# Optimization experiments

Measured on AMD Instinct MI355X. Metric: run time of the kernel, lower is better.

The kernel has to match this reference:

```python
import jax, jax.numpy as jnp
import numpy as np

SCALING = 2.0  # alpha / r = 128 / 64


def setup_inputs() -> dict:
    key = jax.random.key(0)
    k1, k2, k3, k4, k5 = jax.random.split(key, 5)
    B, S, DIN, DOUT, R = 4, 2048, 4096, 4096, 64
    x = jax.random.normal(k1, (B, S, DIN), dtype=jnp.float32)
    # int8 quantized weight codes in [-127, 127] (stored as int32 for portability)
    qweight = jax.random.randint(k2, (DOUT, DIN), -127, 128, dtype=jnp.int32)
    # per-output-row absmax dequant scale (already divided by 127)
    scale = jax.random.uniform(k3, (DOUT, 1), dtype=jnp.float32, minval=0.005, maxval=0.02)
    lora_A = jax.random.normal(k4, (R, DIN), dtype=jnp.float32) * 0.02
    lora_B = jax.random.normal(k5, (DOUT, R), dtype=jnp.float32) * 0.02
    return {"x": x, "qweight": qweight, "scale": scale, "lora_A": lora_A, "lora_B": lora_B}


def reference(x, qweight, scale, lora_A, lora_B):
    # inline int8 dequant: w[o,i] = code[o,i] * scale[o]
    w = qweight.astype(x.dtype) * scale  # [DOUT, DIN]
    base = jnp.einsum('bsi,oi->bso', x, w)
    # low-rank LoRA path: (x @ A^T) @ B^T, scaled
    xa = jnp.einsum('bsi,ri->bsr', x, lora_A)       # [B,S,R]
    lora = jnp.einsum('bsr,or->bso', xa, lora_B)    # [B,S,DOUT]
    return base + SCALING * lora
```

## Files before the change

### kernel.cpp

```cpp
#include <hip/hip_runtime.h>
#include <hip/hip_bf16.h>
#include <stdint.h>


typedef __bf16 bf16x8 __attribute__((ext_vector_type(8)));
typedef float f32x4 __attribute__((ext_vector_type(4)));
typedef int i32x4 __attribute__((ext_vector_type(4)));

#define DIN   4096
#define DOUT  4096
#define MTOT  8192
#define RNK   64
#define NT    64

__device__ inline void gload_lds16(const void* g, void* l) {
  __builtin_amdgcn_global_load_lds((const __attribute__((address_space(1))) void*)g,
                                   (__attribute__((address_space(3))) void*)l,
                                   16, 0, 0);
}

__global__ __launch_bounds__(256) void prep_kernel(const float* __restrict__ x,
                                                   const int* __restrict__ qw,
                                                   const float* __restrict__ lA,
                                                   const float* __restrict__ lB,
                                                   signed char* __restrict__ Xi8,
                                                   float* __restrict__ tstep,
                                                   signed char* __restrict__ Wi8,
                                                   signed char* __restrict__ Ai8,
                                                   float* __restrict__ astep,
                                                   __bf16* __restrict__ Blt) {
  const int bid = blockIdx.x, t = threadIdx.x;
  const float* src = nullptr;
  signed char* dst = nullptr;
  float* stp = nullptr;
  int row = 0;
  if (bid < 8192) { src = x; dst = Xi8; stp = tstep; row = bid; }
  else if (bid < 8256) { src = lA; dst = Ai8; stp = astep; row = bid - 8192; }
  if (src) {
    const float4* xr = (const float4*)(src + (size_t)row * DIN);
    float4 v[4];
    float m = 0.f;
#pragma unroll
    for (int s = 0; s < 4; ++s) {
      v[s] = xr[t + s * 256];
      m = fmaxf(m, fmaxf(fmaxf(fabsf(v[s].x), fabsf(v[s].y)),
                         fmaxf(fabsf(v[s].z), fabsf(v[s].w))));
    }
#pragma unroll
    for (int off = 32; off > 0; off >>= 1) m = fmaxf(m, __shfl_xor(m, off));
    __shared__ float wm[4];
    if ((t & 63) == 0) wm[t >> 6] = m;
    __syncthreads();
    m = fmaxf(fmaxf(wm[0], wm[1]), fmaxf(wm[2], wm[3]));
    m = fmaxf(m, 1e-30f);
    const float rs = 127.0f / m;
    int* orow = (int*)(dst + (size_t)row * DIN);
#pragma unroll
    for (int s = 0; s < 4; ++s) {
      float e[4] = {v[s].x, v[s].y, v[s].z, v[s].w};
      union { signed char c[4]; int i; } p;
#pragma unroll
      for (int j = 0; j < 4; ++j) {
        int q = __float2int_rn(e[j] * rs);
        q = q > 127 ? 127 : (q < -127 ? -127 : q);
        p.c[j] = (signed char)q;
      }
      orow[t + s * 256] = p.i;
    }
    if (t == 0) stp[row] = m * (1.0f / 127.0f);
  } else if (bid < 8512) {
    int i = (bid - 8256) * 256 + t;
    float4 v = ((const float4*)lB)[i];
    union { __bf16 h[4]; uint64_t u; } p;
    p.h[0] = (__bf16)(2.0f * v.x); p.h[1] = (__bf16)(2.0f * v.y);
    p.h[2] = (__bf16)(2.0f * v.z); p.h[3] = (__bf16)(2.0f * v.w);
    ((uint64_t*)Blt)[i] = p.u;
  } else {
    int i = (bid - 8512) * 256 + t;
    int4 v = ((const int4*)qw)[i];
    union { signed char c[4]; int i; } p;
    p.c[0] = (signed char)v.x; p.c[1] = (signed char)v.y;
    p.c[2] = (signed char)v.z; p.c[3] = (signed char)v.w;
    ((int*)Wi8)[i] = p.i;
  }
}

__global__ __launch_bounds__(256) void lora_xa_kernel(const signed char* __restrict__ Xi8,
                                                      const float* __restrict__ tstep,
                                                      const signed char* __restrict__ Ai8,
                                                      const float* __restrict__ astep,
                                                      __bf16* __restrict__ xa) {
  __shared__ i32x4 red[4][64][4];
  const int w = threadIdx.x >> 6, lane = threadIdx.x & 63;
  const int rowbase = blockIdx.x * 16;
  i32x4 acc[4] = {};
  const int k00 = w * 1024 + (lane >> 4) * 16;
  const signed char* xrow = Xi8 + (size_t)(rowbase + (lane & 15)) * DIN + k00;
  const signed char* ab = Ai8 + (size_t)(lane & 15) * DIN + k00;
#pragma unroll 4
  for (int k = 0; k < 1024; k += 64) {
    i32x4 af = *(const i32x4*)(xrow + k);
#pragma unroll
    for (int ni = 0; ni < 4; ++ni) {
      i32x4 bv = *(const i32x4*)(ab + (size_t)ni * 16 * DIN + k);
      acc[ni] = __builtin_amdgcn_mfma_i32_16x16x64_i8(af, bv, acc[ni], 0, 0, 0);
    }
  }
#pragma unroll
  for (int ni = 0; ni < 4; ++ni) red[w][lane][ni] = acc[ni];
  __syncthreads();
  if (w == 0) {
    f32x4 tm = *(const f32x4*)&tstep[rowbase + (lane >> 4) * 4];
#pragma unroll
    for (int ni = 0; ni < 4; ++ni) {
      i32x4 s = red[0][lane][ni];
#pragma unroll
      for (int u = 1; u < 4; ++u) s += red[u][lane][ni];
      const int col = ni * 16 + (lane & 15);
      const float as = astep[col];
#pragma unroll
      for (int j = 0; j < 4; ++j) {
        int row = rowbase + (lane >> 4) * 4 + j;
        xa[(size_t)row * RNK + col] = (__bf16)((float)s[j] * tm[j] * as);
      }
    }
  }
}

__global__ __launch_bounds__(512, 1) void gemm_i8_kernel(const signed char* __restrict__ Xi8,
                                                         const signed char* __restrict__ Wi8,
                                                         const float* __restrict__ scale,
                                                         const float* __restrict__ tstep,
                                                         const __bf16* __restrict__ xa,
                                                         const __bf16* __restrict__ Blt,
                                                         float* __restrict__ out) {
  extern __shared__ char smem[];
  const int tid = threadIdx.x;
  const int lane = tid & 63;
  const int w = tid >> 6;
  const int wr = w >> 2;
  const int wc = w & 3;

  const int swz = (blockIdx.x & 7) * 64 + (blockIdx.x >> 3);
  const int bx = swz & 15;
  const int by = swz >> 4;
  const size_t bm = (size_t)by * 256, bn = (size_t)bx * 256;

  const int rc = ((lane >> 4) ^ ((lane >> 1) & 3)) << 4;
  const int srow = tid >> 2;
  const int scol = ((tid & 3) ^ ((tid >> 3) & 3)) << 4;

  auto SH = [&](const signed char* g, size_t r0, int srct, int ldsoff) {
    gload_lds16(g + (r0 + srow) * (size_t)4096 + srct * 64 + scol,
                smem + ldsoff + tid * 16);
  };
  auto stage = [&](int srct, int buf) {
    int b = buf * 32768;
    SH(Xi8, bm, srct, b); SH(Xi8, bm + 128, srct, b + 8192);
    SH(Wi8, bn, srct, b + 16384); SH(Wi8, bn + 128, srct, b + 24576);
  };

  i32x4 aP[4], bP[4], aQ[4], bQ[4], a2[4];
  i32x4 acc[8][4] = {};

  stage(0, 0); stage(1, 1); stage(2, 2);
  asm volatile("s_waitcnt vmcnt(4)" ::: "memory");
  __builtin_amdgcn_s_barrier();
  {
    const int ab0 = wr * 8192 + (lane & 15) * 64 + rc;
    const int bb0 = 16384 + (wc >> 1) * 8192 + (wc & 1) * 4096 + (lane & 15) * 64 + rc;
#pragma unroll
    for (int mi = 0; mi < 4; ++mi) aP[mi] = *(const i32x4*)(smem + ab0 + mi * 1024);
#pragma unroll
    for (int ni = 0; ni < 4; ++ni) bP[ni] = *(const i32x4*)(smem + bb0 + ni * 1024);
  }

  auto body = [&](int kt, auto& ac, auto& bc, auto& an, auto& bn) {
    const int bufb = (kt & 3) * 32768;
    const int ab = bufb + wr * 8192 + (lane & 15) * 64 + rc;
    const int st = (kt + 3 < NT) ? kt + 3 : NT - 1;
    stage(st, (kt + 3) & 3);
#pragma unroll
    for (int mi = 0; mi < 4; ++mi)
      a2[mi] = *(const i32x4*)(smem + ab + 4096 + mi * 1024);
#pragma unroll
    for (int mi = 0; mi < 4; ++mi)
#pragma unroll
      for (int ni = 0; ni < 4; ++ni)
        acc[mi][ni] = __builtin_amdgcn_mfma_i32_16x16x64_i8(ac[mi], bc[ni], acc[mi][ni], 0, 0, 0);
    const int nbufb = ((kt + 1) & 3) * 32768;
    const int nab = nbufb + wr * 8192 + (lane & 15) * 64 + rc;
    const int nbb = nbufb + 16384 + (wc >> 1) * 8192 + (wc & 1) * 4096 + (lane & 15) * 64 + rc;
#pragma unroll
    for (int mi = 0; mi < 4; ++mi) an[mi] = *(const i32x4*)(smem + nab + mi * 1024);
#pragma unroll
    for (int ni = 0; ni < 4; ++ni) bn[ni] = *(const i32x4*)(smem + nbb + ni * 1024);
#pragma unroll
    for (int mi = 0; mi < 4; ++mi)
#pragma unroll
      for (int ni = 0; ni < 4; ++ni)
        acc[4 + mi][ni] = __builtin_amdgcn_mfma_i32_16x16x64_i8(a2[mi], bc[ni], acc[4 + mi][ni], 0, 0, 0);
    __builtin_amdgcn_sched_barrier(0);
    asm volatile("s_waitcnt vmcnt(4)" ::: "memory");
    __builtin_amdgcn_s_barrier();
  };

  for (int kt = 0; kt < NT; kt += 2) {
    body(kt, aP, bP, aQ, bQ);
    body(kt + 1, aQ, bQ, aP, bP);
  }

  const int sl_row = lane >> 3;
  const int sl_col = ((lane & 7) ^ (lane >> 3)) << 4;
  auto SBF = [&](const __bf16* g, size_t r0, int ldsoff) {
    char* d0 = smem + ldsoff + w * 2048 + lane * 16;
#pragma unroll
    for (int s = 0; s < 2; ++s) {
      const int rl = (w * 2 + s) * 8 + sl_row;
      gload_lds16((const char*)g + (r0 + rl) * 128 + sl_col, d0 + s * 1024);
    }
  };
  SBF(xa, bm, 0); SBF(xa, bm + 128, 16384);
  SBF(Blt, bn, 32768); SBF(Blt, bn + 128, 49152);

  float sc[4];
#pragma unroll
  for (int ni = 0; ni < 4; ++ni)
    sc[ni] = scale[bn + wc * 64 + ni * 16 + (lane & 15)];
  f32x4 tm[8];
#pragma unroll
  for (int mi = 0; mi < 8; ++mi)
    tm[mi] = *(const f32x4*)&tstep[bm + wr * 128 + mi * 16 + (lane >> 4) * 4];

  asm volatile("s_waitcnt vmcnt(0)" ::: "memory");
  __builtin_amdgcn_s_barrier();

  const int cx0 = ((lane >> 4) << 4) ^ ((lane & 7) << 4);
  const int cx1 = (64 | ((lane >> 4) << 4)) ^ ((lane & 7) << 4);
  const int abE = wr * 16384 + (lane & 15) * 128;
  const int bbE = 32768 + (wc >> 1) * 16384 + ((wc & 1) * 64 + (lane & 15)) * 128;

  bf16x8 bl0[4], bl1[4];
#pragma unroll
  for (int ni = 0; ni < 4; ++ni) {
    bl0[ni] = *(const bf16x8*)(smem + bbE + ni * 2048 + cx0);
    bl1[ni] = *(const bf16x8*)(smem + bbE + ni * 2048 + cx1);
  }
#pragma unroll
  for (int mi = 0; mi < 8; ++mi) {
    bf16x8 ax0 = *(const bf16x8*)(smem + abE + mi * 2048 + cx0);
    bf16x8 ax1 = *(const bf16x8*)(smem + abE + mi * 2048 + cx1);
    const size_t row = bm + wr * 128 + mi * 16 + (lane >> 4) * 4;
#pragma unroll
    for (int ni = 0; ni < 4; ++ni) {
      f32x4 l = {0.f, 0.f, 0.f, 0.f};
      l = __builtin_amdgcn_mfma_f32_16x16x32_bf16(ax0, bl0[ni], l, 0, 0, 0);
      l = __builtin_amdgcn_mfma_f32_16x16x32_bf16(ax1, bl1[ni], l, 0, 0, 0);
      const size_t col = bn + wc * 64 + ni * 16 + (lane & 15);
#pragma unroll
      for (int j = 0; j < 4; ++j)
        out[(row + j) * DOUT + col] = (float)acc[mi][ni][j] * (sc[ni] * tm[mi][j]) + l[j];
    }
  }
}

extern "C" void kernel_launch(void* const* d_in, const int* in_sizes, int n_in,
                              void* d_out, int out_size, void* d_ws, size_t ws_size,
                              hipStream_t stream) {
  const float* x = (const float*)d_in[0];
  const int* qw = (const int*)d_in[1];
  const float* scale = (const float*)d_in[2];
  const float* lA = (const float*)d_in[3];
  const float* lB = (const float*)d_in[4];
  float* out = (float*)d_out;

  char* ws = (char*)d_ws;
  signed char* Xi8 = (signed char*)ws;
  signed char* Wi8 = (signed char*)(ws + 33554432);
  __bf16* xa    = (__bf16*)(ws + 50331648);
  signed char* Ai8 = (signed char*)(ws + 51380224);
  __bf16* Blt   = (__bf16*)(ws + 51904512);
  float* tstep  = (float*)(ws + 52428800);
  float* astep  = (float*)(ws + 52461568);

  hipFuncSetAttribute((const void*)gemm_i8_kernel,
                      hipFuncAttributeMaxDynamicSharedMemorySize, 131072);

  prep_kernel<<<24896, 256, 0, stream>>>(x, qw, lA, lB, Xi8, tstep, Wi8, Ai8, astep, Blt);
  lora_xa_kernel<<<MTOT / 16, 256, 0, stream>>>(Xi8, tstep, Ai8, astep, xa);
  gemm_i8_kernel<<<(MTOT / 256) * (DOUT / 256), 512, 131072, stream>>>(
      Xi8, Wi8, scale, tstep, xa, Blt, out);
}
```

Measured before the change: 198.9 us.

## Halve GEMM workgroup to four waves, each computing a 128x128 tile

The int8 GEMM kernel drops from 8 waves to 4 waves per 256x256 block. Each wave now holds an 8x8 grid of 16x16 int32 accumulators (128x128 outputs). The LDS staging loop and the epilogue LoRA fragment loads are reorganised to match. This raises MFMA work per LDS fragment load and cuts the number of waves at the barrier. In exchange it needs far more accumulator registers, which risks spills or AGPR pressure, and leaves fewer waves to hide latency.

```diff
diff --git a/kernel.cpp b/kernel.cpp
--- a/kernel.cpp
+++ b/kernel.cpp
@@ -127,7 +127,7 @@
   }
 }
 
-__global__ __launch_bounds__(512, 1) void gemm_i8_kernel(const signed char* __restrict__ Xi8,
+__global__ __launch_bounds__(256, 1) void gemm_i8_kernel(const signed char* __restrict__ Xi8,
                                                          const signed char* __restrict__ Wi8,
                                                          const float* __restrict__ scale,
                                                          const float* __restrict__ tstep,
@@ -138,8 +138,8 @@
   const int tid = threadIdx.x;
   const int lane = tid & 63;
   const int w = tid >> 6;
-  const int wr = w >> 2;
-  const int wc = w & 3;
+  const int wr = w >> 1;
+  const int wc = w & 1;
 
   const int swz = (blockIdx.x & 7) * 64 + (blockIdx.x >> 3);
   const int bx = swz & 15;
@@ -150,58 +150,50 @@
   const int srow = tid >> 2;
   const int scol = ((tid & 3) ^ ((tid >> 3) & 3)) << 4;
 
-  auto SH = [&](const signed char* g, size_t r0, int srct, int ldsoff) {
-    gload_lds16(g + (r0 + srow) * (size_t)4096 + srct * 64 + scol,
-                smem + ldsoff + tid * 16);
-  };
   auto stage = [&](int srct, int buf) {
     int b = buf * 32768;
-    SH(Xi8, bm, srct, b); SH(Xi8, bm + 128, srct, b + 8192);
-    SH(Wi8, bn, srct, b + 16384); SH(Wi8, bn + 128, srct, b + 24576);
+#pragma unroll
+    for (int i = 0; i < 4; ++i)
+      gload_lds16(Xi8 + (bm + 64 * i + srow) * (size_t)4096 + srct * 64 + scol,
+                  smem + b + i * 4096 + tid * 16);
+#pragma unroll
+    for (int i = 0; i < 4; ++i)
+      gload_lds16(Wi8 + (bn + 64 * i + srow) * (size_t)4096 + srct * 64 + scol,
+                  smem + b + 16384 + i * 4096 + tid * 16);
   };
 
-  i32x4 aP[4], bP[4], aQ[4], bQ[4], a2[4];
-  i32x4 acc[8][4] = {};
+  const int aoff = wr * 8192 + (lane & 15) * 64 + rc;
+  const int boff = 16384 + wc * 8192 + (lane & 15) * 64 + rc;
+
+  i32x4 aP[8], bP[8], aQ[8], bQ[8];
+  i32x4 acc[8][8] = {};
 
   stage(0, 0); stage(1, 1); stage(2, 2);
-  asm volatile("s_waitcnt vmcnt(4)" ::: "memory");
+  asm volatile("s_waitcnt vmcnt(8)" ::: "memory");
   __builtin_amdgcn_s_barrier();
-  {
-    const int ab0 = wr * 8192 + (lane & 15) * 64 + rc;
-    const int bb0 = 16384 + (wc >> 1) * 8192 + (wc & 1) * 4096 + (lane & 15) * 64 + rc;
-#pragma unroll
-    for (int mi = 0; mi < 4; ++mi) aP[mi] = *(const i32x4*)(smem + ab0 + mi * 1024);
-#pragma unroll
-    for (int ni = 0; ni < 4; ++ni) bP[ni] = *(const i32x4*)(smem + bb0 + ni * 1024);
-  }
-
-  auto body = [&](int kt, auto& ac, auto& bc, auto& an, auto& bn) {
-    const int bufb = (kt & 3) * 32768;
-    const int ab = bufb + wr * 8192 + (lane & 15) * 64 + rc;
+#pragma unroll
+  for (int mi = 0; mi < 8; ++mi) aP[mi] = *(const i32x4*)(smem + aoff + mi * 1024);
+#pragma unroll
+  for (int ni = 0; ni < 8; ++ni) bP[ni] = *(const i32x4*)(smem + boff + ni * 1024);
+
+  auto body = [&](int kt, i32x4 (&aC)[8], i32x4 (&bC)[8],
+                  i32x4 (&aN)[8], i32x4 (&bN)[8]) {
     const int st = (kt + 3 < NT) ? kt + 3 : NT - 1;
     stage(st, (kt + 3) & 3);
-#pragma unroll
-    for (int mi = 0; mi < 4; ++mi)
-      a2[mi] = *(const i32x4*)(smem + ab + 4096 + mi * 1024);
-#pragma unroll
-    for (int mi = 0; mi < 4; ++mi)
-#pragma unroll
-      for (int ni = 0; ni < 4; ++ni)
-        acc[mi][ni] = __builtin_amdgcn_mfma_i32_16x16x64_i8(ac[mi], bc[ni], acc[mi][ni], 0, 0, 0);
-    const int nbufb = ((kt + 1) & 3) * 32768;
-    const int nab = nbufb + wr * 8192 + (lane & 15) * 64 + rc;
-    const int nbb = nbufb + 16384 + (wc >> 1) * 8192 + (wc & 1) * 4096 + (lane & 15) * 64 + rc;
-#pragma unroll
-    for (int mi = 0; mi < 4; ++mi) an[mi] = *(const i32x4*)(smem + nab + mi * 1024);
-#pragma unroll
-    for (int ni = 0; ni < 4; ++ni) bn[ni] = *(const i32x4*)(smem + nbb + ni * 1024);
-#pragma unroll
-    for (int mi = 0; mi < 4; ++mi)
-#pragma unroll
-      for (int ni = 0; ni < 4; ++ni)
-        acc[4 + mi][ni] = __builtin_amdgcn_mfma_i32_16x16x64_i8(a2[mi], bc[ni], acc[4 + mi][ni], 0, 0, 0);
+    if (kt + 1 < NT) {
+      const int nb = ((kt + 1) & 3) * 32768;
+#pragma unroll
+      for (int mi = 0; mi < 8; ++mi) aN[mi] = *(const i32x4*)(smem + nb + aoff + mi * 1024);
+#pragma unroll
+      for (int ni = 0; ni < 8; ++ni) bN[ni] = *(const i32x4*)(smem + nb + boff + ni * 1024);
+    }
+#pragma unroll
+    for (int mi = 0; mi < 8; ++mi)
+#pragma unroll
+      for (int ni = 0; ni < 8; ++ni)
+        acc[mi][ni] = __builtin_amdgcn_mfma_i32_16x16x64_i8(aC[mi], bC[ni], acc[mi][ni], 0, 0, 0);
     __builtin_amdgcn_sched_barrier(0);
-    asm volatile("s_waitcnt vmcnt(4)" ::: "memory");
+    asm volatile("s_waitcnt vmcnt(8)" ::: "memory");
     __builtin_amdgcn_s_barrier();
   };
 
@@ -210,23 +202,23 @@
     body(kt + 1, aQ, bQ, aP, bP);
   }
 
-  const int sl_row = lane >> 3;
-  const int sl_col = ((lane & 7) ^ (lane >> 3)) << 4;
-  auto SBF = [&](const __bf16* g, size_t r0, int ldsoff) {
-    char* d0 = smem + ldsoff + w * 2048 + lane * 16;
-#pragma unroll
-    for (int s = 0; s < 2; ++s) {
-      const int rl = (w * 2 + s) * 8 + sl_row;
-      gload_lds16((const char*)g + (r0 + rl) * 128 + sl_col, d0 + s * 1024);
-    }
-  };
-  SBF(xa, bm, 0); SBF(xa, bm + 128, 16384);
-  SBF(Blt, bn, 32768); SBF(Blt, bn + 128, 49152);
-
-  float sc[4];
-#pragma unroll
-  for (int ni = 0; ni < 4; ++ni)
-    sc[ni] = scale[bn + wc * 64 + ni * 16 + (lane & 15)];
+  asm volatile("s_waitcnt vmcnt(0)" ::: "memory");
+  __builtin_amdgcn_s_barrier();
+  const int erow = tid >> 3;
+  const int ecol = (((tid & 7) ^ ((tid >> 3) & 7)) << 4);
+#pragma unroll
+  for (int i = 0; i < 8; ++i)
+    gload_lds16((const char*)xa + (bm + 32 * i + erow) * 128 + ecol,
+                smem + i * 4096 + tid * 16);
+#pragma unroll
+  for (int i = 0; i < 8; ++i)
+    gload_lds16((const char*)Blt + (bn + 32 * i + erow) * 128 + ecol,
+                smem + 32768 + i * 4096 + tid * 16);
+
+  float sc[8];
+#pragma unroll
+  for (int ni = 0; ni < 8; ++ni)
+    sc[ni] = scale[bn + wc * 128 + ni * 16 + (lane & 15)];
   f32x4 tm[8];
 #pragma unroll
   for (int mi = 0; mi < 8; ++mi)
@@ -238,25 +230,21 @@
   const int cx0 = ((lane >> 4) << 4) ^ ((lane & 7) << 4);
   const int cx1 = (64 | ((lane >> 4) << 4)) ^ ((lane & 7) << 4);
   const int abE = wr * 16384 + (lane & 15) * 128;
-  const int bbE = 32768 + (wc >> 1) * 16384 + ((wc & 1) * 64 + (lane & 15)) * 128;
-
-  bf16x8 bl0[4], bl1[4];
-#pragma unroll
-  for (int ni = 0; ni < 4; ++ni) {
-    bl0[ni] = *(const bf16x8*)(smem + bbE + ni * 2048 + cx0);
-    bl1[ni] = *(const bf16x8*)(smem + bbE + ni * 2048 + cx1);
-  }
+  const int bbE = 32768 + wc * 16384 + (lane & 15) * 128;
+
 #pragma unroll
   for (int mi = 0; mi < 8; ++mi) {
     bf16x8 ax0 = *(const bf16x8*)(smem + abE + mi * 2048 + cx0);
     bf16x8 ax1 = *(const bf16x8*)(smem + abE + mi * 2048 + cx1);
     const size_t row = bm + wr * 128 + mi * 16 + (lane >> 4) * 4;
 #pragma unroll
-    for (int ni = 0; ni < 4; ++ni) {
+    for (int ni = 0; ni < 8; ++ni) {
+      bf16x8 bl0 = *(const bf16x8*)(smem + bbE + ni * 2048 + cx0);
+      bf16x8 bl1 = *(const bf16x8*)(smem + bbE + ni * 2048 + cx1);
       f32x4 l = {0.f, 0.f, 0.f, 0.f};
-      l = __builtin_amdgcn_mfma_f32_16x16x32_bf16(ax0, bl0[ni], l, 0, 0, 0);
-      l = __builtin_amdgcn_mfma_f32_16x16x32_bf16(ax1, bl1[ni], l, 0, 0, 0);
-      const size_t col = bn + wc * 64 + ni * 16 + (lane & 15);
+      l = __builtin_amdgcn_mfma_f32_16x16x32_bf16(ax0, bl0, l, 0, 0, 0);
+      l = __builtin_amdgcn_mfma_f32_16x16x32_bf16(ax1, bl1, l, 0, 0, 0);
+      const size_t col = bn + wc * 128 + ni * 16 + (lane & 15);
 #pragma unroll
       for (int j = 0; j < 4; ++j)
         out[(row + j) * DOUT + col] = (float)acc[mi][ni][j] * (sc[ni] * tm[mi][j]) + l[j];
@@ -288,6 +276,6 @@
 
   prep_kernel<<<24896, 256, 0, stream>>>(x, qw, lA, lB, Xi8, tstep, Wi8, Ai8, astep, Blt);
   lora_xa_kernel<<<MTOT / 16, 256, 0, stream>>>(Xi8, tstep, Ai8, astep, xa);
-  gemm_i8_kernel<<<(MTOT / 256) * (DOUT / 256), 512, 131072, stream>>>(
+  gemm_i8_kernel<<<(MTOT / 256) * (DOUT / 256), 256, 131072, stream>>>(
       Xi8, Wi8, scale, tstep, xa, Blt, out);
 }
```

Result: slower. 615.0 us (+209.2%).

## Defer upper-half MFMAs to next iteration to overlap LDS operand loads

Applied to the files above, without the earlier changes.

Restructures the int8 GEMM main loop into a skewed software pipeline. The second block of MFMAs for each k-tile now runs at the start of the next iteration, so the LDS reads of the next tile's A/B fragments and the upper-half A fragments are issued before the lower-half MFMAs rather than between them. It adds a second register set for the upper A fragments, an explicit lgkmcnt(0) wait, a prologue and epilogue iteration, and a final vmcnt(0) barrier before the LoRA stage. The extra registers may raise VGPR pressure and affect occupancy.

```diff
diff --git a/kernel.cpp b/kernel.cpp
--- a/kernel.cpp
+++ b/kernel.cpp
@@ -160,55 +160,68 @@
     SH(Wi8, bn, srct, b + 16384); SH(Wi8, bn + 128, srct, b + 24576);
   };
 
-  i32x4 aP[4], bP[4], aQ[4], bQ[4], a2[4];
+  const int aoffw = wr * 8192 + (lane & 15) * 64 + rc;
+  const int boffw = 16384 + (wc >> 1) * 8192 + (wc & 1) * 4096 + (lane & 15) * 64 + rc;
+
+  i32x4 aP[4], bP[4], aQ[4], bQ[4], a2P[4], a2Q[4];
   i32x4 acc[8][4] = {};
 
   stage(0, 0); stage(1, 1); stage(2, 2);
   asm volatile("s_waitcnt vmcnt(4)" ::: "memory");
   __builtin_amdgcn_s_barrier();
-  {
-    const int ab0 = wr * 8192 + (lane & 15) * 64 + rc;
-    const int bb0 = 16384 + (wc >> 1) * 8192 + (wc & 1) * 4096 + (lane & 15) * 64 + rc;
-#pragma unroll
-    for (int mi = 0; mi < 4; ++mi) aP[mi] = *(const i32x4*)(smem + ab0 + mi * 1024);
-#pragma unroll
-    for (int ni = 0; ni < 4; ++ni) bP[ni] = *(const i32x4*)(smem + bb0 + ni * 1024);
-  }
-
-  auto body = [&](int kt, auto& ac, auto& bc, auto& an, auto& bn) {
-    const int bufb = (kt & 3) * 32768;
-    const int ab = bufb + wr * 8192 + (lane & 15) * 64 + rc;
+#pragma unroll
+  for (int mi = 0; mi < 4; ++mi) aP[mi] = *(const i32x4*)(smem + aoffw + mi * 1024);
+#pragma unroll
+  for (int ni = 0; ni < 4; ++ni) bP[ni] = *(const i32x4*)(smem + boffw + ni * 1024);
+
+  auto body = [&](int kt, i32x4 (&AY)[4], i32x4 (&BY)[4],
+                  i32x4 (&AX)[4], i32x4 (&BX)[4],
+                  i32x4 (&a2Y)[4], i32x4 (&a2X)[4], bool doHi) {
+    if (doHi) {
+#pragma unroll
+      for (int mi = 0; mi < 4; ++mi)
+#pragma unroll
+        for (int ni = 0; ni < 4; ++ni)
+          acc[4 + mi][ni] = __builtin_amdgcn_mfma_i32_16x16x64_i8(a2X[mi], BX[ni], acc[4 + mi][ni], 0, 0, 0);
+    }
     const int st = (kt + 3 < NT) ? kt + 3 : NT - 1;
     stage(st, (kt + 3) & 3);
+    const int ab = (kt & 3) * 32768 + aoffw;
 #pragma unroll
     for (int mi = 0; mi < 4; ++mi)
-      a2[mi] = *(const i32x4*)(smem + ab + 4096 + mi * 1024);
+      a2Y[mi] = *(const i32x4*)(smem + ab + 4096 + mi * 1024);
+    if (kt + 1 < NT) {
+      const int nb = ((kt + 1) & 3) * 32768;
+#pragma unroll
+      for (int mi = 0; mi < 4; ++mi) AX[mi] = *(const i32x4*)(smem + nb + aoffw + mi * 1024);
+#pragma unroll
+      for (int ni = 0; ni < 4; ++ni) BX[ni] = *(const i32x4*)(smem + nb + boffw + ni * 1024);
+    }
 #pragma unroll
     for (int mi = 0; mi < 4; ++mi)
 #pragma unroll
       for (int ni = 0; ni < 4; ++ni)
-        acc[mi][ni] = __builtin_amdgcn_mfma_i32_16x16x64_i8(ac[mi], bc[ni], acc[mi][ni], 0, 0, 0);
-    const int nbufb = ((kt + 1) & 3) * 32768;
-    const int nab = nbufb + wr * 8192 + (lane & 15) * 64 + rc;
-    const int nbb = nbufb + 16384 + (wc >> 1) * 8192 + (wc & 1) * 4096 + (lane & 15) * 64 + rc;
-#pragma unroll
-    for (int mi = 0; mi < 4; ++mi) an[mi] = *(const i32x4*)(smem + nab + mi * 1024);
-#pragma unroll
-    for (int ni = 0; ni < 4; ++ni) bn[ni] = *(const i32x4*)(smem + nbb + ni * 1024);
-#pragma unroll
-    for (int mi = 0; mi < 4; ++mi)
-#pragma unroll
-      for (int ni = 0; ni < 4; ++ni)
-        acc[4 + mi][ni] = __builtin_amdgcn_mfma_i32_16x16x64_i8(a2[mi], bc[ni], acc[4 + mi][ni], 0, 0, 0);
+        acc[mi][ni] = __builtin_amdgcn_mfma_i32_16x16x64_i8(AY[mi], BY[ni], acc[mi][ni], 0, 0, 0);
+    asm volatile("s_waitcnt lgkmcnt(0)" ::: "memory");
     __builtin_amdgcn_sched_barrier(0);
     asm volatile("s_waitcnt vmcnt(4)" ::: "memory");
     __builtin_amdgcn_s_barrier();
   };
 
-  for (int kt = 0; kt < NT; kt += 2) {
-    body(kt, aP, bP, aQ, bQ);
-    body(kt + 1, aQ, bQ, aP, bP);
-  }
+  body(0, aP, bP, aQ, bQ, a2P, a2Q, false);
+  for (int kt = 1; kt < NT - 1; kt += 2) {
+    body(kt, aQ, bQ, aP, bP, a2Q, a2P, true);
+    body(kt + 1, aP, bP, aQ, bQ, a2P, a2Q, true);
+  }
+  body(NT - 1, aQ, bQ, aP, bP, a2Q, a2P, true);
+#pragma unroll
+  for (int mi = 0; mi < 4; ++mi)
+#pragma unroll
+    for (int ni = 0; ni < 4; ++ni)
+      acc[4 + mi][ni] = __builtin_amdgcn_mfma_i32_16x16x64_i8(a2Q[mi], bQ[ni], acc[4 + mi][ni], 0, 0, 0);
+
+  asm volatile("s_waitcnt vmcnt(0)" ::: "memory");
+  __builtin_amdgcn_s_barrier();
 
   const int sl_row = lane >> 3;
   const int sl_col = ((lane & 7) ^ (lane >> 3)) << 4;
```

Result: no change. 198.1 us, median of 2 (-0.4%).
